# Optimization experiments

Measured on AMD Instinct MI355X. Metric: run time of the kernel, lower is better.

## Reference

```python
import jax, jax.numpy as jnp
import numpy as np

CANVAS_SIZE = 224
N_SEGMENTS = 4
N_SAMPLES = 50
SOFTNESS = 0.02


def setup_inputs() -> dict:
    key = jax.random.key(0)
    k1, k2 = jax.random.split(key)
    n_paths = 1024
    paths_control_points = jax.random.uniform(k1, (n_paths, N_SEGMENTS, 4, 2), dtype=jnp.float32)
    colors = jax.random.uniform(k2, (n_paths, 4), dtype=jnp.float32)
    return {"paths_control_points": paths_control_points, "colors": colors}


def reference(paths_control_points, colors):
    H = W = CANVAS_SIZE
    n_paths = paths_control_points.shape[0]

    # Cubic Bezier basis at t in linspace(0,1,50)[:-1]  -> (49, 4)
    t = jnp.linspace(0.0, 1.0, N_SAMPLES)[:-1]
    mt = 1.0 - t
    basis = jnp.stack([mt**3, 3.0 * mt**2 * t, 3.0 * mt * t**2, t**3], axis=-1)

    # Sample all curve points for all paths/segments at once: (P, S, T, 2)
    pts = jnp.einsum('tc,psce->pste', basis, paths_control_points)
    pts = pts.reshape(n_paths, -1, 2)  # (P, S*T, 2) == (P, 196, 2)

    center = pts.mean(axis=1)  # (P, 2) -> (x, y)
    avg_radius = jnp.linalg.norm(pts - center[:, None, :], axis=-1).mean(axis=1)  # (P,)

    # Pixel grid in [0,1], 'ij' indexing: grid_y varies over rows, grid_x over cols
    lin = jnp.linspace(0.0, 1.0, H)
    grid_y, grid_x = jnp.meshgrid(lin, lin, indexing='ij')  # (H, W) each

    # Distance field per path: (P, H, W)
    dx = grid_x[None] - center[:, 0, None, None]
    dy = grid_y[None] - center[:, 1, None, None]
    dist = jnp.sqrt(dx * dx + dy * dy)

    # Soft disk mask scaled by per-path alpha: (P, H, W)
    masks = jax.nn.sigmoid((avg_radius[:, None, None] - dist) / SOFTNESS)
    masks = masks * colors[:, 3, None, None]

    # Sequential front-to-back alpha compositing (order matters) via scan
    canvas0 = jnp.ones((3, H, W), dtype=paths_control_points.dtype)

    def step(canvas, xs):
        m, c = xs  # m: (H, W), c: (3,)
        canvas = canvas * (1.0 - m)[None] + c[:, None, None] * m[None]
        return canvas, None

    canvas, _ = jax.lax.scan(step, canvas0, (masks, colors[:, :3]))
    return canvas
```

## Files before the change

### kernel.cpp

```cpp
#include <hip/hip_runtime.h>
#include <math.h>

#define NPATHS   1024
#define CANVAS_H 224
#define CANVAS_W 224
#define NPIX     (CANVAS_H * CANVAS_W)
#define NSAMP    49
#define K2EXP    72.134752f

#define NWAVES   16
#define PPW      (NPATHS / NWAVES)


__device__ __forceinline__ float sf(int v) { return __int_as_float(v); }

__global__ __launch_bounds__(64) void path_setup_kernel(
    const float* __restrict__ cps,
    const float* __restrict__ colors,
    float* __restrict__ pd)
{
    const int tid = blockIdx.x * 64 + threadIdx.x;
    const int p = tid >> 2;
    const int s = tid & 3;

    const float4* cp4 = reinterpret_cast<const float4*>(cps);
    float4 a = cp4[p * 8 + s * 2];
    float4 b = cp4[p * 8 + s * 2 + 1];

    float sx = 0.0f, sy = 0.0f;
    for (int i = 0; i < NSAMP; ++i) {
        float t  = (float)i * (1.0f / 49.0f);
        float mt = 1.0f - t;
        float b0 = mt * mt * mt;
        float b1 = 3.0f * mt * mt * t;
        float b2 = 3.0f * mt * t * t;
        float b3 = t * t * t;
        sx += b0 * a.x + b1 * a.z + b2 * b.x + b3 * b.z;
        sy += b0 * a.y + b1 * a.w + b2 * b.y + b3 * b.w;
    }
    sx += __shfl_xor(sx, 1); sx += __shfl_xor(sx, 2);
    sy += __shfl_xor(sy, 1); sy += __shfl_xor(sy, 2);
    const float inv_n = 1.0f / 196.0f;
    float cx = sx * inv_n;
    float cy = sy * inv_n;

    float sr = 0.0f;
    for (int i = 0; i < NSAMP; ++i) {
        float t  = (float)i * (1.0f / 49.0f);
        float mt = 1.0f - t;
        float b0 = mt * mt * mt;
        float b1 = 3.0f * mt * mt * t;
        float b2 = 3.0f * mt * t * t;
        float b3 = t * t * t;
        float ptx = b0 * a.x + b1 * a.z + b2 * b.x + b3 * b.z;
        float pty = b0 * a.y + b1 * a.w + b2 * b.y + b3 * b.w;
        float dx = ptx - cx;
        float dy = pty - cy;
        sr += sqrtf(dx * dx + dy * dy);
    }
    sr += __shfl_xor(sr, 1); sr += __shfl_xor(sr, 2);
    float r = sr * inv_n;

    if (s == 0) {
        float4 col = reinterpret_cast<const float4*>(colors)[p];
        float4* o = reinterpret_cast<float4*>(pd) + (size_t)p * 2;
        o[0] = make_float4(cx * K2EXP, cy * K2EXP, -K2EXP * r, col.w);
        o[1] = make_float4(col.x * col.w, col.y * col.w, col.z * col.w, 0.0f);
    }
}

__global__ __launch_bounds__(1024) void render_kernel(
    const float* __restrict__ pd,
    float* __restrict__ out)
{
    __shared__ float4 lds[NPATHS * 2];

    {
        const float4* src = reinterpret_cast<const float4*>(pd);
        lds[threadIdx.x]        = src[threadIdx.x];
        lds[threadIdx.x + 1024] = src[threadIdx.x + 1024];
    }
    __syncthreads();

    const int wave = __builtin_amdgcn_readfirstlane((int)(threadIdx.x >> 6));
    const int lane = threadIdx.x & 63;
    const int lx = lane & 15;
    const int lq = lane >> 4;
    const int xx  = blockIdx.x * 16 + lx;
    const int yy0 = blockIdx.y * 8 + lq;
    const float pxs  = (float)xx * (K2EXP / 223.0f);
    const float py0s = (float)yy0 * (K2EXP / 223.0f);
    const float py1s = (float)(yy0 + 4) * (K2EXP / 223.0f);

    const float4* plds = lds + wave * (PPW * 2);

    float T0 = 1.0f, Ar0 = 0.0f, Ag0 = 0.0f, Ab0 = 0.0f;
    float T1 = 1.0f, Ar1 = 0.0f, Ag1 = 0.0f, Ab1 = 0.0f;

#pragma unroll 4
    for (int p = 0; p < PPW; ++p) {
        float4 d0 = plds[2 * p];
        float4 d1 = plds[2 * p + 1];
        float dx  = pxs - d0.x;
        float dy0 = py0s - d0.y;
        float dy1 = py1s - d0.y;
        float dx2 = dx * dx;
        float d20 = __builtin_fmaf(dy0, dy0, dx2);
        float d21 = __builtin_fmaf(dy1, dy1, dx2);
        float s0 = __builtin_amdgcn_sqrtf(d20);
        float s1 = __builtin_amdgcn_sqrtf(d21);
        float e0 = __builtin_amdgcn_exp2f(s0 + d0.z);
        float e1 = __builtin_amdgcn_exp2f(s1 + d0.z);
        float q0 = __builtin_amdgcn_rcpf(1.0f + e0);
        float q1 = __builtin_amdgcn_rcpf(1.0f + e1);
        float om0 = __builtin_fmaf(-d0.w, q0, 1.0f);
        float om1 = __builtin_fmaf(-d0.w, q1, 1.0f);
        T0 *= om0;
        T1 *= om1;
        Ar0 = __builtin_fmaf(Ar0, om0, d1.x * q0);
        Ag0 = __builtin_fmaf(Ag0, om0, d1.y * q0);
        Ab0 = __builtin_fmaf(Ab0, om0, d1.z * q0);
        Ar1 = __builtin_fmaf(Ar1, om1, d1.x * q1);
        Ag1 = __builtin_fmaf(Ag1, om1, d1.y * q1);
        Ab1 = __builtin_fmaf(Ab1, om1, d1.z * q1);
    }

    __syncthreads();
    lds[wave * 128 + lane]      = make_float4(T0, Ar0, Ag0, Ab0);
    lds[wave * 128 + 64 + lane] = make_float4(T1, Ar1, Ag1, Ab1);
    __syncthreads();

    if (wave == 0) {
#pragma unroll
        for (int sub = 0; sub < 2; ++sub) {
            float R = 1.0f, G = 1.0f, Bb = 1.0f;
#pragma unroll
            for (int w = 0; w < NWAVES; ++w) {
                float4 c = lds[w * 128 + sub * 64 + lane];
                R  = __builtin_fmaf(R,  c.x, c.y);
                G  = __builtin_fmaf(G,  c.x, c.z);
                Bb = __builtin_fmaf(Bb, c.x, c.w);
            }
            const int pix = (yy0 + sub * 4) * CANVAS_W + xx;
            out[pix]            = R;
            out[NPIX + pix]     = G;
            out[2 * NPIX + pix] = Bb;
        }
    }
}

extern "C" void kernel_launch(void* const* d_in, const int* in_sizes, int n_in,
                              void* d_out, int out_size, void* d_ws, size_t ws_size,
                              hipStream_t stream) {
    const float* cps    = (const float*)d_in[0];
    const float* colors = (const float*)d_in[1];
    float* out = (float*)d_out;
    float* pd  = (float*)d_ws;

    path_setup_kernel<<<(NPATHS * 4) / 64, 64, 0, stream>>>(cps, colors, pd);

    dim3 grid(CANVAS_W / 16, CANVAS_H / 8);
    render_kernel<<<grid, 1024, 0, stream>>>(pd, out);
}
```

Before: 44.38 us.

## Cull distant paths per wave and split rendering into chunked partials plus combine pass

Adds a per-path cull radius (radius plus margin, squared) so a wave skips the sqrt/exp/rcp compositing math when no lane is inside the path's influence region. Rendering is restructured into small 128-thread blocks over a 3D grid that each write per-chunk partial transmittance/color to workspace, followed by a separate combine kernel. The cull treats a path's contribution as exactly zero beyond the margin (sigmoid tail), which introduces a small approximation error. It also adds a 16x canvas-sized float4 workspace round trip and an extra launch, and falls back to the original LDS kernel if the workspace is too small.

After: 45.09 us. No clear change (+1.6%).

```diff
diff --git a/kernel.cpp b/kernel.cpp
--- a/kernel.cpp
+++ b/kernel.cpp
@@ -7,12 +7,11 @@
 #define NPIX     (CANVAS_H * CANVAS_W)
 #define NSAMP    49
 #define K2EXP    72.134752f
-
-#define NWAVES   16
-#define PPW      (NPATHS / NWAVES)
-
-
-__device__ __forceinline__ float sf(int v) { return __int_as_float(v); }
+#define CULL_MARGIN 0.22f
+
+#define CHUNKS   16
+#define CPP      (NPATHS / CHUNKS)
+
 
 __global__ __launch_bounds__(64) void path_setup_kernel(
     const float* __restrict__ cps,
@@ -63,18 +62,95 @@
 
     if (s == 0) {
         float4 col = reinterpret_cast<const float4*>(colors)[p];
+        float rc = K2EXP * (r + CULL_MARGIN);
         float4* o = reinterpret_cast<float4*>(pd) + (size_t)p * 2;
-        o[0] = make_float4(cx * K2EXP, cy * K2EXP, -K2EXP * r, col.w);
-        o[1] = make_float4(col.x * col.w, col.y * col.w, col.z * col.w, 0.0f);
-    }
-}
-
-__global__ __launch_bounds__(1024) void render_kernel(
+        o[0] = make_float4(cx * K2EXP, cy * K2EXP, -K2EXP * r, rc * rc);
+        o[1] = make_float4(col.x * col.w, col.y * col.w, col.z * col.w, col.w);
+    }
+}
+
+__global__ __launch_bounds__(128) void render_kernel(
+    const float* __restrict__ pd,
+    float4* __restrict__ cb)
+{
+    const int wave = __builtin_amdgcn_readfirstlane((int)(threadIdx.x >> 6));
+    const int lane = threadIdx.x & 63;
+    const int chunk = blockIdx.x * 2 + wave;
+    const int lx = lane & 15;
+    const int lq = lane >> 4;
+    const int xx  = blockIdx.y * 16 + lx;
+    const int yy0 = blockIdx.z * 8 + lq;
+    const float pxs  = (float)xx * (K2EXP / 223.0f);
+    const float py0s = (float)yy0 * (K2EXP / 223.0f);
+    const float py1s = (float)(yy0 + 4) * (K2EXP / 223.0f);
+
+    const float4* __restrict__ pdv =
+        reinterpret_cast<const float4*>(pd) + (size_t)chunk * (CPP * 2);
+
+    float T0 = 1.0f, Ar0 = 0.0f, Ag0 = 0.0f, Ab0 = 0.0f;
+    float T1 = 1.0f, Ar1 = 0.0f, Ag1 = 0.0f, Ab1 = 0.0f;
+
+#pragma unroll 2
+    for (int p = 0; p < CPP; ++p) {
+        float4 d0 = pdv[2 * p];
+        float4 d1 = pdv[2 * p + 1];
+        float dx  = pxs - d0.x;
+        float dy0 = py0s - d0.y;
+        float dy1 = py1s - d0.y;
+        float dx2 = dx * dx;
+        float d20 = __builtin_fmaf(dy0, dy0, dx2);
+        float d21 = __builtin_fmaf(dy1, dy1, dx2);
+        float dmin = fminf(d20, d21);
+        if (__any(dmin < d0.w)) {
+            float s0 = __builtin_amdgcn_sqrtf(d20);
+            float s1 = __builtin_amdgcn_sqrtf(d21);
+            float e0 = __builtin_amdgcn_exp2f(s0 + d0.z);
+            float e1 = __builtin_amdgcn_exp2f(s1 + d0.z);
+            float q0 = __builtin_amdgcn_rcpf(1.0f + e0);
+            float q1 = __builtin_amdgcn_rcpf(1.0f + e1);
+            float om0 = __builtin_fmaf(-d1.w, q0, 1.0f);
+            float om1 = __builtin_fmaf(-d1.w, q1, 1.0f);
+            T0 *= om0;
+            T1 *= om1;
+            Ar0 = __builtin_fmaf(Ar0, om0, d1.x * q0);
+            Ag0 = __builtin_fmaf(Ag0, om0, d1.y * q0);
+            Ab0 = __builtin_fmaf(Ab0, om0, d1.z * q0);
+            Ar1 = __builtin_fmaf(Ar1, om1, d1.x * q1);
+            Ag1 = __builtin_fmaf(Ag1, om1, d1.y * q1);
+            Ab1 = __builtin_fmaf(Ab1, om1, d1.z * q1);
+        }
+    }
+
+    const int pix0 = yy0 * CANVAS_W + xx;
+    const int pix1 = (yy0 + 4) * CANVAS_W + xx;
+    float4* row = cb + (size_t)chunk * NPIX;
+    row[pix0] = make_float4(T0, Ar0, Ag0, Ab0);
+    row[pix1] = make_float4(T1, Ar1, Ag1, Ab1);
+}
+
+__global__ __launch_bounds__(256) void combine_kernel(
+    const float4* __restrict__ cb,
+    float* __restrict__ out)
+{
+    int pix = blockIdx.x * 256 + threadIdx.x;
+    float R = 1.0f, G = 1.0f, B = 1.0f;
+#pragma unroll
+    for (int k = 0; k < CHUNKS; ++k) {
+        float4 w = cb[(size_t)k * NPIX + pix];
+        R = __builtin_fmaf(R, w.x, w.y);
+        G = __builtin_fmaf(G, w.x, w.z);
+        B = __builtin_fmaf(B, w.x, w.w);
+    }
+    out[pix]            = R;
+    out[NPIX + pix]     = G;
+    out[2 * NPIX + pix] = B;
+}
+
+__global__ __launch_bounds__(1024) void render_direct_kernel(
     const float* __restrict__ pd,
     float* __restrict__ out)
 {
     __shared__ float4 lds[NPATHS * 2];
-
     {
         const float4* src = reinterpret_cast<const float4*>(pd);
         lds[threadIdx.x]        = src[threadIdx.x];
@@ -92,13 +168,13 @@
     const float py0s = (float)yy0 * (K2EXP / 223.0f);
     const float py1s = (float)(yy0 + 4) * (K2EXP / 223.0f);
 
-    const float4* plds = lds + wave * (PPW * 2);
+    const float4* plds = lds + wave * (CPP * 2);
 
     float T0 = 1.0f, Ar0 = 0.0f, Ag0 = 0.0f, Ab0 = 0.0f;
     float T1 = 1.0f, Ar1 = 0.0f, Ag1 = 0.0f, Ab1 = 0.0f;
 
 #pragma unroll 4
-    for (int p = 0; p < PPW; ++p) {
+    for (int p = 0; p < CPP; ++p) {
         float4 d0 = plds[2 * p];
         float4 d1 = plds[2 * p + 1];
         float dx  = pxs - d0.x;
@@ -113,10 +189,9 @@
         float e1 = __builtin_amdgcn_exp2f(s1 + d0.z);
         float q0 = __builtin_amdgcn_rcpf(1.0f + e0);
         float q1 = __builtin_amdgcn_rcpf(1.0f + e1);
-        float om0 = __builtin_fmaf(-d0.w, q0, 1.0f);
-        float om1 = __builtin_fmaf(-d0.w, q1, 1.0f);
-        T0 *= om0;
-        T1 *= om1;
+        float om0 = __builtin_fmaf(-d1.w, q0, 1.0f);
+        float om1 = __builtin_fmaf(-d1.w, q1, 1.0f);
+        T0 *= om0; T1 *= om1;
         Ar0 = __builtin_fmaf(Ar0, om0, d1.x * q0);
         Ag0 = __builtin_fmaf(Ag0, om0, d1.y * q0);
         Ab0 = __builtin_fmaf(Ab0, om0, d1.z * q0);
@@ -135,7 +210,7 @@
         for (int sub = 0; sub < 2; ++sub) {
             float R = 1.0f, G = 1.0f, Bb = 1.0f;
 #pragma unroll
-            for (int w = 0; w < NWAVES; ++w) {
+            for (int w = 0; w < 16; ++w) {
                 float4 c = lds[w * 128 + sub * 64 + lane];
                 R  = __builtin_fmaf(R,  c.x, c.y);
                 G  = __builtin_fmaf(G,  c.x, c.z);
@@ -159,6 +234,15 @@
 
     path_setup_kernel<<<(NPATHS * 4) / 64, 64, 0, stream>>>(cps, colors, pd);
 
-    dim3 grid(CANVAS_W / 16, CANVAS_H / 8);
-    render_kernel<<<grid, 1024, 0, stream>>>(pd, out);
-}
+    const size_t PD_BYTES = (size_t)NPATHS * 8 * 4;
+    const size_t CB_BYTES = (size_t)CHUNKS * NPIX * 16;
+    if (ws_size >= PD_BYTES + CB_BYTES) {
+        float4* cb = reinterpret_cast<float4*>((char*)d_ws + PD_BYTES);
+        dim3 grid(CHUNKS / 2, CANVAS_W / 16, CANVAS_H / 8);
+        render_kernel<<<grid, 128, 0, stream>>>(pd, cb);
+        combine_kernel<<<NPIX / 256, 256, 0, stream>>>(cb, out);
+    } else {
+        dim3 grid(CANVAS_W / 16, CANVAS_H / 8);
+        render_direct_kernel<<<grid, 1024, 0, stream>>>(pd, out);
+    }
+}
```
